# Kernel optimization log

Measured on AMD Instinct MI355X. Metric: run time of the kernel, lower is better.

## Reference

```python
import jax, jax.numpy as jnp
import numpy as np

N_HEADS = 16


def setup_inputs() -> dict:
    key = jax.random.key(0)
    ks = jax.random.split(key, 4)
    B, S, E = 4, 2048, 1024
    x = jax.random.normal(ks[0], (B, S, E), dtype=jnp.float32)
    w_attn = jax.random.normal(ks[1], (E, 3 * E), dtype=jnp.float32) * 0.02
    b_attn = jnp.zeros((3 * E,), dtype=jnp.float32)
    w_proj = jax.random.normal(ks[2], (E, E), dtype=jnp.float32) * 0.02
    b_proj = jnp.zeros((E,), dtype=jnp.float32)
    return {"x": x, "w_attn": w_attn, "b_attn": b_attn, "w_proj": w_proj, "b_proj": b_proj}


def reference(x, w_attn, b_attn, w_proj, b_proj):
    B, S, E = x.shape
    H = N_HEADS
    D = E // H
    # fused QKV projection (Conv1D: x @ W + b)
    qkv = x @ w_attn + b_attn                     # [B, S, 3E]
    q, k, v = jnp.split(qkv, 3, axis=-1)          # each [B, S, E]
    q = q.reshape(B, S, H, D).transpose(0, 2, 1, 3)  # [B, H, S, D]
    k = k.reshape(B, S, H, D).transpose(0, 2, 1, 3)
    v = v.reshape(B, S, H, D).transpose(0, 2, 1, 3)
    # scaled QK^T
    scores = jnp.einsum('bhqd,bhkd->bhqk', q, k) / jnp.sqrt(jnp.asarray(D, dtype=x.dtype))
    # causal mask via where with dtype-min fill (matches torch.where(c_m, w, finfo.min))
    causal = jnp.tril(jnp.ones((S, S), dtype=bool))  # [S, S]
    scores = jnp.where(causal[None, None, :, :], scores, jnp.finfo(scores.dtype).min)
    attn = jax.nn.softmax(scores, axis=-1)        # [B, H, S, S]
    o = jnp.einsum('bhqk,bhkd->bhqd', attn, v)    # [B, H, S, D]
    o = o.transpose(0, 2, 1, 3).reshape(B, S, E)  # merge heads
    return o @ w_proj + b_proj                    # output projection
```

## Files before the change

kernel.cpp:

```cpp
#include <hip/hip_runtime.h>
#include <stdint.h>


typedef __bf16 bf16;
typedef __bf16 bf16x4 __attribute__((ext_vector_type(4)));
typedef __bf16 bf16x8 __attribute__((ext_vector_type(8)));
typedef float  f32x4  __attribute__((ext_vector_type(4)));

#define DEV __device__ __forceinline__

DEV void async_copy16(bf16* lds, const bf16* g) {
  __builtin_amdgcn_global_load_lds(
      (__attribute__((address_space(1))) void*)(uintptr_t)g,
      (__attribute__((address_space(3))) void*)(uint32_t)(uintptr_t)lds,
      16, 0, 0);
}

__global__ __launch_bounds__(256) void cast_x_kernel(const float* __restrict__ in,
                                                     bf16* __restrict__ out, int n4) {
  int i = blockIdx.x * blockDim.x + threadIdx.x;
  int stride = gridDim.x * blockDim.x;
  for (; i < n4; i += stride) {
    float4 v = ((const float4*)in)[i];
    bf16x4 o = { (bf16)v.x, (bf16)v.y, (bf16)v.z, (bf16)v.w };
    *(bf16x4*)(out + (size_t)i * 4) = o;
  }
}

__global__ __launch_bounds__(256) void transpose_cast_kernel(const float* __restrict__ W,
                                                             bf16* __restrict__ Wt,
                                                             int Kd, int Nd) {
  __shared__ alignas(16) bf16 T[64 * 80];
  const int t = threadIdx.x;
  const int n0 = blockIdx.x * 64;
  const int k0 = blockIdx.y * 64;
#pragma unroll
  for (int i = 0; i < 4; ++i) {
    int idx = t + i * 256;
    int r  = idx >> 4;
    int c4 = (idx & 15) * 4;
    float4 v = *(const float4*)(W + (size_t)(k0 + r) * Nd + n0 + c4);
    bf16x4 o = { (bf16)v.x, (bf16)v.y, (bf16)v.z, (bf16)v.w };
    *(bf16x4*)(&T[r * 80 + c4]) = o;
  }
  __syncthreads();
#pragma unroll
  for (int i = 0; i < 2; ++i) {
    int idx = t + i * 256;
    int n = idx >> 3;
    int c = idx & 7;
    bf16x8 o;
#pragma unroll
    for (int j = 0; j < 8; ++j) o[j] = T[(c * 8 + j) * 80 + n];
    *(bf16x8*)(Wt + (size_t)(n0 + n) * Kd + k0 + c * 8) = o;
  }
}

__global__ __launch_bounds__(256) void vtrans_kernel(const bf16* __restrict__ qkv,
                                                     bf16* __restrict__ vt) {
  __shared__ alignas(16) bf16 T[64 * 80];
  const int t  = threadIdx.x;
  const int s0 = blockIdx.x * 64;
  const int bh = blockIdx.y;
  const int b = bh >> 4, h = bh & 15;
#pragma unroll
  for (int i = 0; i < 2; ++i) {
    int idx = t + i * 256;
    int s = idx >> 3, c = idx & 7;
    bf16x8 v = *(const bf16x8*)(qkv + (size_t)(b * 2048 + s0 + s) * 3072 + 2048 + h * 64 + c * 8);
    *(bf16x8*)(&T[s * 80 + c * 8]) = v;
  }
  __syncthreads();
#pragma unroll
  for (int i = 0; i < 2; ++i) {
    int idx = t + i * 256;
    int d = idx >> 3, c = idx & 7;
    bf16x8 o;
#pragma unroll
    for (int j = 0; j < 8; ++j) {
      int pos = c * 8 + j;
      int key = (pos & 32) | (((pos >> 2) & 1) << 4) | (((pos >> 3) & 3) << 2) | (pos & 3);
      o[j] = T[key * 80 + d];
    }
    *(bf16x8*)(vt + (size_t)(bh * 64 + d) * 2048 + s0 + c * 8) = o;
  }
}

template <typename OutT>
__global__ __launch_bounds__(512, 4) void gemm256_kernel(const bf16* __restrict__ A,
                                                         const bf16* __restrict__ Bt,
                                                         const float* __restrict__ bias,
                                                         OutT* __restrict__ C,
                                                         int M, int N, int K,
                                                         float qscale, int qcols,
                                                         int nbx) {
  __shared__ alignas(16) bf16 As[3][256 * 32];
  __shared__ alignas(16) bf16 Bs[3][128 * 32];

  const int tid  = threadIdx.x;
  const int lane = tid & 63;
  const int w    = tid >> 6;
  const int wm = w >> 1, wn = w & 1;
  const int l15 = lane & 15, l16 = lane >> 4;

  const int nwg = (int)gridDim.x;
  const int cpx = nwg >> 3;
  const int swz = ((int)blockIdx.x & 7) * cpx + ((int)blockIdx.x >> 3);
  const int m0 = (swz / nbx) * 256;
  const int n0 = (swz % nbx) * 128;

  const int c0  = w * 64 + lane;
  const int rA0 = c0 >> 2, sA0 = c0 & 3;
  const int rA1 = rA0 + 128;
  const bf16* srcA0 = A  + (size_t)(m0 + rA0) * K + 8 * (sA0 ^ ((rA0 >> 1) & 3));
  const bf16* srcA1 = A  + (size_t)(m0 + rA1) * K + 8 * (sA0 ^ ((rA1 >> 1) & 3));
  const bf16* srcB  = Bt + (size_t)(n0 + rA0) * K + 8 * (sA0 ^ ((rA0 >> 1) & 3));

#define STAGE_TILE(buf, kt)                                       \
  {                                                               \
    const int k0_ = (kt) * 32;                                    \
    async_copy16(&As[buf][(w * 64) * 8],         srcA0 + k0_);    \
    async_copy16(&As[buf][(512 + w * 64) * 8],   srcA1 + k0_);    \
    async_copy16(&Bs[buf][(w * 64) * 8],         srcB  + k0_);    \
  }

  f32x4 acc[4][4];
  f32x4 zf = {0.f, 0.f, 0.f, 0.f};
#pragma unroll
  for (int i = 0; i < 4; ++i)
#pragma unroll
    for (int j = 0; j < 4; ++j) acc[i][j] = zf;

  const int KT = K >> 5;
  STAGE_TILE(0, 0)
  STAGE_TILE(1, 1)

  const int soff = 8 * (l16 ^ ((l15 >> 1) & 3));

  int bufc = 0;
  int bufs = 2;
  for (int kt = 0; kt < KT; ++kt) {
    if (kt < KT - 1) { asm volatile("s_waitcnt vmcnt(3)" ::: "memory"); }
    else             { asm volatile("s_waitcnt vmcnt(0)" ::: "memory"); }
    __builtin_amdgcn_s_barrier();
    asm volatile("" ::: "memory");
    if (kt + 2 < KT) STAGE_TILE(bufs, kt + 2)

    bf16x8 bfr[4], afr[4];
#pragma unroll
    for (int n = 0; n < 4; ++n) {
      int rb = wn * 64 + n * 16 + l15;
      bfr[n] = *(const bf16x8*)(&Bs[bufc][rb * 32 + soff]);
    }
#pragma unroll
    for (int m = 0; m < 4; ++m) {
      int ra = wm * 64 + m * 16 + l15;
      afr[m] = *(const bf16x8*)(&As[bufc][ra * 32 + soff]);
    }
    __builtin_amdgcn_s_setprio(1);
#pragma unroll
    for (int m = 0; m < 4; ++m)
#pragma unroll
      for (int n = 0; n < 4; ++n)
        acc[m][n] = __builtin_amdgcn_mfma_f32_16x16x32_bf16(afr[m], bfr[n], acc[m][n], 0, 0, 0);
    __builtin_amdgcn_s_setprio(0);
    asm volatile("" ::: "memory");
    bufc = (bufc == 2) ? 0 : bufc + 1;
    bufs = (bufs == 2) ? 0 : bufs + 1;
  }

#pragma unroll
  for (int n = 0; n < 4; ++n) {
    int col = n0 + wn * 64 + n * 16 + l15;
    float bb = bias[col];
    float sc2 = (col < qcols) ? qscale : 1.0f;
#pragma unroll
    for (int m = 0; m < 4; ++m) {
#pragma unroll
      for (int reg = 0; reg < 4; ++reg) {
        int row = m0 + wm * 64 + m * 16 + l16 * 4 + reg;
        C[(size_t)row * N + col] = (OutT)((acc[m][n][reg] + bb) * sc2);
      }
    }
  }
#undef STAGE_TILE
}

__global__ __launch_bounds__(512, 4) void flash_kernel(const bf16* __restrict__ qkv,
                                                       const bf16* __restrict__ vt,
                                                       bf16* __restrict__ obuf) {
  constexpr int S = 2048, E3 = 3072;
  __shared__ alignas(16) bf16 Ks[2][64 * 64];
  __shared__ alignas(16) bf16 Vs[2][64 * 64];

  const int tid  = threadIdx.x;
  const int lane = tid & 63;
  const int w    = tid >> 6;
  const int bx = blockIdx.x;
  const int bh = blockIdx.y;
  const int b = bh >> 4, h = bh & 15;
  const int l15 = lane & 15, l16 = lane >> 4;

  const int sr  = w * 8 + (lane >> 3);
  const int scc = lane & 7;
  const bf16* kstage = qkv + (size_t)(b * S + sr) * E3 + 1024 + h * 64 + 8 * (scc ^ (sr & 7));
  const bf16* vstage = vt + (size_t)(bh * 64 + sr) * S + 8 * (scc ^ (sr & 7));

  const int xsw = l15 & 7;
  const uint32_t rdA = (uint32_t)(l15 * 128 + 16 * (l16 ^ xsw));
  const uint32_t rdB = (uint32_t)(l15 * 128 + 16 * ((4 + l16) ^ xsw));

#define KV_STAGE(buf, kv0_)                                        \
  {                                                                \
    async_copy16(Ks[buf] + w * 512, kstage + (size_t)(kv0_) * E3); \
    async_copy16(Vs[buf] + w * 512, vstage + (kv0_));              \
  }

  for (int half = 0; half < 2; ++half) {
    const int t = half ? (15 - bx) : bx;
    const int q0 = t * 128;
    const int wq0 = q0 + w * 16;
    const int nsteps = 2 * t + 2;

    KV_STAGE(0, 0)

    bf16x8 qf[2];
    {
      const bf16* qbase = qkv + (size_t)(b * S + wq0 + l15) * E3 + h * 64;
#pragma unroll
      for (int dk = 0; dk < 2; ++dk)
        qf[dk] = *(const bf16x8*)(qbase + (dk * 4 + l16) * 8);
    }

    float lstate = 0.f;
    f32x4 oacc[4];
    f32x4 zf = {0.f, 0.f, 0.f, 0.f};
#pragma unroll
    for (int i = 0; i < 4; ++i) oacc[i] = zf;

    __syncthreads();

#define FLASH_STEP(CUR, STEPIDX)                                                  \
    {                                                                             \
      const int kv0 = (STEPIDX) * 64;                                             \
      if ((STEPIDX) + 1 < nsteps) KV_STAGE((CUR) ^ 1, kv0 + 64)                   \
      if (kv0 <= wq0 + 15) {                     \
        f32x4 sv[4];                                                              \
        _Pragma("unroll")                                                         \
        for (int kf = 0; kf < 4; ++kf) sv[kf] = zf;                               \
        __builtin_amdgcn_s_setprio(1);                                            \
        _Pragma("unroll")                                                         \
        for (int kf = 0; kf < 4; ++kf) {                                          \
          bf16x8 k0 = *(const bf16x8*)((const char*)Ks[CUR] + rdA + kf * 2048);   \
          sv[kf] = __builtin_amdgcn_mfma_f32_16x16x32_bf16(k0, qf[0], sv[kf], 0, 0, 0); \
          bf16x8 k1 = *(const bf16x8*)((const char*)Ks[CUR] + rdB + kf * 2048);   \
          sv[kf] = __builtin_amdgcn_mfma_f32_16x16x32_bf16(k1, qf[1], sv[kf], 0, 0, 0); \
        }                                                                         \
        __builtin_amdgcn_s_setprio(0);                                            \
        if (kv0 + 63 > wq0) {     \
          const int qrow_ = wq0 + l15;                                            \
          _Pragma("unroll")                                                       \
          for (int kf = 0; kf < 4; ++kf)                                          \
            _Pragma("unroll")                                                     \
            for (int reg = 0; reg < 4; ++reg) {                                   \
              int key = kv0 + kf * 16 + l16 * 4 + reg;                            \
              if (key > qrow_) sv[kf][reg] = -1e30f;                              \
            }                                                                     \
        }                                                                         \
        float rsum = 0.f;                                                         \
        _Pragma("unroll")                                                         \
        for (int kf = 0; kf < 4; ++kf)                                            \
          _Pragma("unroll")                                                       \
          for (int reg = 0; reg < 4; ++reg) {                                     \
            float p = __builtin_amdgcn_exp2f(sv[kf][reg]);                        \
            sv[kf][reg] = p;                                                      \
            rsum += p;                                                            \
          }                                                                       \
        rsum += __shfl_xor(rsum, 16);                                             \
        rsum += __shfl_xor(rsum, 32);                                             \
        lstate += rsum;                                                           \
             \
        bf16x8 pb[2];                                                             \
        _Pragma("unroll")                                                         \
        for (int kc = 0; kc < 2; ++kc) {                                          \
          bf16x8 tq;                                                              \
          tq[0] = (bf16)sv[2 * kc][0];  tq[1] = (bf16)sv[2 * kc][1];              \
          tq[2] = (bf16)sv[2 * kc][2];  tq[3] = (bf16)sv[2 * kc][3];              \
          tq[4] = (bf16)sv[2 * kc + 1][0]; tq[5] = (bf16)sv[2 * kc + 1][1];       \
          tq[6] = (bf16)sv[2 * kc + 1][2]; tq[7] = (bf16)sv[2 * kc + 1][3];       \
          pb[kc] = tq;                                                            \
        }                                                                         \
        __builtin_amdgcn_s_setprio(1);                                            \
        _Pragma("unroll")                                                         \
        for (int nf = 0; nf < 4; ++nf) {                                          \
          bf16x8 vf0 = *(const bf16x8*)((const char*)Vs[CUR] + rdA + nf * 2048);  \
          oacc[nf] = __builtin_amdgcn_mfma_f32_16x16x32_bf16(vf0, pb[0], oacc[nf], 0, 0, 0); \
          bf16x8 vf1 = *(const bf16x8*)((const char*)Vs[CUR] + rdB + nf * 2048);  \
          oacc[nf] = __builtin_amdgcn_mfma_f32_16x16x32_bf16(vf1, pb[1], oacc[nf], 0, 0, 0); \
        }                                                                         \
        __builtin_amdgcn_s_setprio(0);                                            \
      }                                                                           \
      __syncthreads();          \
    }

    for (int step = 0; step < nsteps; step += 2) {
      FLASH_STEP(0, step)
      FLASH_STEP(1, step + 1)
    }
#undef FLASH_STEP

    float inv = 1.0f / lstate;
    int qrow = wq0 + l15;
#pragma unroll
    for (int nf = 0; nf < 4; ++nf) {
      bf16x4 o4 = { (bf16)(oacc[nf][0] * inv), (bf16)(oacc[nf][1] * inv),
                    (bf16)(oacc[nf][2] * inv), (bf16)(oacc[nf][3] * inv) };
      *(bf16x4*)(obuf + (size_t)(b * S + qrow) * 1024 + h * 64 + nf * 16 + l16 * 4) = o4;
    }
  }
#undef KV_STAGE
}

extern "C" void kernel_launch(void* const* d_in, const int* in_sizes, int n_in,
                              void* d_out, int out_size, void* d_ws, size_t ws_size,
                              hipStream_t stream) {
  (void)in_sizes; (void)n_in; (void)out_size; (void)ws_size;
  const float* x      = (const float*)d_in[0];
  const float* w_attn = (const float*)d_in[1];
  const float* b_attn = (const float*)d_in[2];
  const float* w_proj = (const float*)d_in[3];
  const float* b_proj = (const float*)d_in[4];
  float* out = (float*)d_out;

  char* ws = (char*)d_ws;
  bf16* xb  = (bf16*)(ws + 0);
  bf16* wat = (bf16*)(ws + 16777216);
  bf16* wpt = (bf16*)(ws + 23068672);
  bf16* qkv = (bf16*)(ws + 25165824);
  bf16* vt  = (bf16*)(ws + 75497472);
  bf16* ob  = (bf16*)(ws + 92274688);

  const float QSCALE = 0.18033688011112042f;

  cast_x_kernel<<<2048, 256, 0, stream>>>(x, xb, 8192 * 1024 / 4);
  transpose_cast_kernel<<<dim3(48, 16), 256, 0, stream>>>(w_attn, wat, 1024, 3072);
  transpose_cast_kernel<<<dim3(16, 16), 256, 0, stream>>>(w_proj, wpt, 1024, 1024);
  gemm256_kernel<bf16><<<768, 512, 0, stream>>>(xb, wat, b_attn, qkv,
                                                8192, 3072, 1024, QSCALE, 1024, 24);
  vtrans_kernel<<<dim3(32, 64), 256, 0, stream>>>(qkv, vt);
  flash_kernel<<<dim3(8, 64), 512, 0, stream>>>(qkv, vt, ob);
  gemm256_kernel<float><<<256, 512, 0, stream>>>(ob, wpt, b_proj, out,
                                                 8192, 1024, 1024, 1.0f, 0, 8);
}
```

Baseline: 160.8 us.

## Double query rows per flash wave to reuse K/V tiles across two sub-tiles

Each flash block now covers 256 query rows, with every wave handling two 16-row query sub-tiles against the same K/V LDS tiles. Each K/V load and barrier is amortized over twice the MFMA work, and the grid is halved. In exchange, register pressure rises (launch bounds lowered to 2 blocks/CU), occupancy falls, and causal tail waste per block grows.

```diff
diff --git a/kernel.cpp b/kernel.cpp
--- a/kernel.cpp
+++ b/kernel.cpp
@@ -186,7 +186,7 @@
 #undef STAGE_TILE
 }
 
-__global__ __launch_bounds__(512, 4) void flash_kernel(const bf16* __restrict__ qkv,
+__global__ __launch_bounds__(512, 2) void flash_kernel(const bf16* __restrict__ qkv,
                                                        const bf16* __restrict__ vt,
                                                        bf16* __restrict__ obuf) {
   constexpr int S = 2048, E3 = 3072;
@@ -217,26 +217,30 @@
   }
 
   for (int half = 0; half < 2; ++half) {
-    const int t = half ? (15 - bx) : bx;
-    const int q0 = t * 128;
-    const int wq0 = q0 + w * 16;
-    const int nsteps = 2 * t + 2;
+    const int t = half ? (7 - bx) : bx;
+    const int q0 = t * 256;
+    const int wq0 = q0 + w * 32;
+    const int nsteps = 4 * t + 4;
 
     KV_STAGE(0, 0)
 
-    bf16x8 qf[2];
+    bf16x8 qf[2][2];
     {
-      const bf16* qbase = qkv + (size_t)(b * S + wq0 + l15) * E3 + h * 64;
-#pragma unroll
-      for (int dk = 0; dk < 2; ++dk)
-        qf[dk] = *(const bf16x8*)(qbase + (dk * 4 + l16) * 8);
-    }
-
-    float lstate = 0.f;
-    f32x4 oacc[4];
+      const bf16* qbase = qkv + (size_t)(b * S + wq0) * E3 + h * 64;
+#pragma unroll
+      for (int s = 0; s < 2; ++s)
+#pragma unroll
+        for (int dk = 0; dk < 2; ++dk)
+          qf[s][dk] = *(const bf16x8*)(qbase + (size_t)(s * 16 + l15) * E3 + (dk * 4 + l16) * 8);
+    }
+
+    float lstate[2] = {0.f, 0.f};
+    f32x4 oacc[2][4];
     f32x4 zf = {0.f, 0.f, 0.f, 0.f};
 #pragma unroll
-    for (int i = 0; i < 4; ++i) oacc[i] = zf;
+    for (int s = 0; s < 2; ++s)
+#pragma unroll
+      for (int i = 0; i < 4; ++i) oacc[s][i] = zf;
 
     __syncthreads();
 
@@ -244,59 +248,65 @@
     {                                                                             \
       const int kv0 = (STEPIDX) * 64;                                             \
       if ((STEPIDX) + 1 < nsteps) KV_STAGE((CUR) ^ 1, kv0 + 64)                   \
-      if (kv0 <= wq0 + 15) {                     \
-        f32x4 sv[4];                                                              \
+      if (kv0 <= wq0 + 31) {                     \
+        f32x4 sv[2][4];                                                           \
         _Pragma("unroll")                                                         \
-        for (int kf = 0; kf < 4; ++kf) sv[kf] = zf;                               \
+        for (int kf = 0; kf < 4; ++kf) { sv[0][kf] = zf; sv[1][kf] = zf; }        \
         __builtin_amdgcn_s_setprio(1);                                            \
         _Pragma("unroll")                                                         \
         for (int kf = 0; kf < 4; ++kf) {                                          \
           bf16x8 k0 = *(const bf16x8*)((const char*)Ks[CUR] + rdA + kf * 2048);   \
-          sv[kf] = __builtin_amdgcn_mfma_f32_16x16x32_bf16(k0, qf[0], sv[kf], 0, 0, 0); \
+          sv[0][kf] = __builtin_amdgcn_mfma_f32_16x16x32_bf16(k0, qf[0][0], sv[0][kf], 0, 0, 0); \
+          sv[1][kf] = __builtin_amdgcn_mfma_f32_16x16x32_bf16(k0, qf[1][0], sv[1][kf], 0, 0, 0); \
           bf16x8 k1 = *(const bf16x8*)((const char*)Ks[CUR] + rdB + kf * 2048);   \
-          sv[kf] = __builtin_amdgcn_mfma_f32_16x16x32_bf16(k1, qf[1], sv[kf], 0, 0, 0); \
+          sv[0][kf] = __builtin_amdgcn_mfma_f32_16x16x32_bf16(k1, qf[0][1], sv[0][kf], 0, 0, 0); \
+          sv[1][kf] = __builtin_amdgcn_mfma_f32_16x16x32_bf16(k1, qf[1][1], sv[1][kf], 0, 0, 0); \
         }                                                                         \
         __builtin_amdgcn_s_setprio(0);                                            \
-        if (kv0 + 63 > wq0) {     \
-          const int qrow_ = wq0 + l15;                                            \
+        bf16x8 pb[2][2];                                                          \
+        _Pragma("unroll")                                                         \
+        for (int s = 0; s < 2; ++s) {                                             \
+          if (kv0 + 63 > wq0 + s * 16) {                \
+            const int qrow_ = wq0 + s * 16 + l15;                                 \
+            _Pragma("unroll")                                                     \
+            for (int kf = 0; kf < 4; ++kf)                                        \
+              _Pragma("unroll")                                                   \
+              for (int reg = 0; reg < 4; ++reg) {                                 \
+                int key = kv0 + kf * 16 + l16 * 4 + reg;                          \
+                if (key > qrow_) sv[s][kf][reg] = -1e30f;                         \
+              }                                                                   \
+          }                                                                       \
+          float rsum = 0.f;                                                       \
           _Pragma("unroll")                                                       \
           for (int kf = 0; kf < 4; ++kf)                                          \
             _Pragma("unroll")                                                     \
             for (int reg = 0; reg < 4; ++reg) {                                   \
-              int key = kv0 + kf * 16 + l16 * 4 + reg;                            \
-              if (key > qrow_) sv[kf][reg] = -1e30f;                              \
+              float p = __builtin_amdgcn_exp2f(sv[s][kf][reg]);                   \
+              sv[s][kf][reg] = p;                                                 \
+              rsum += p;                                                          \
             }                                                                     \
-        }                                                                         \
-        float rsum = 0.f;                                                         \
-        _Pragma("unroll")                                                         \
-        for (int kf = 0; kf < 4; ++kf)                                            \
+          rsum += __shfl_xor(rsum, 16);                                           \
+          rsum += __shfl_xor(rsum, 32);                                           \
+          lstate[s] += rsum;                                                      \
           _Pragma("unroll")                                                       \
-          for (int reg = 0; reg < 4; ++reg) {                                     \
-            float p = __builtin_amdgcn_exp2f(sv[kf][reg]);                        \
-            sv[kf][reg] = p;                                                      \
-            rsum += p;                                                            \
+          for (int kc = 0; kc < 2; ++kc) {                                        \
+            bf16x8 tq;                                                            \
+            tq[0] = (bf16)sv[s][2 * kc][0];  tq[1] = (bf16)sv[s][2 * kc][1];      \
+            tq[2] = (bf16)sv[s][2 * kc][2];  tq[3] = (bf16)sv[s][2 * kc][3];      \
+            tq[4] = (bf16)sv[s][2 * kc + 1][0]; tq[5] = (bf16)sv[s][2 * kc + 1][1]; \
+            tq[6] = (bf16)sv[s][2 * kc + 1][2]; tq[7] = (bf16)sv[s][2 * kc + 1][3]; \
+            pb[s][kc] = tq;                                                       \
           }                                                                       \
-        rsum += __shfl_xor(rsum, 16);                                             \
-        rsum += __shfl_xor(rsum, 32);                                             \
-        lstate += rsum;                                                           \
-             \
-        bf16x8 pb[2];                                                             \
-        _Pragma("unroll")                                                         \
-        for (int kc = 0; kc < 2; ++kc) {                                          \
-          bf16x8 tq;                                                              \
-          tq[0] = (bf16)sv[2 * kc][0];  tq[1] = (bf16)sv[2 * kc][1];              \
-          tq[2] = (bf16)sv[2 * kc][2];  tq[3] = (bf16)sv[2 * kc][3];              \
-          tq[4] = (bf16)sv[2 * kc + 1][0]; tq[5] = (bf16)sv[2 * kc + 1][1];       \
-          tq[6] = (bf16)sv[2 * kc + 1][2]; tq[7] = (bf16)sv[2 * kc + 1][3];       \
-          pb[kc] = tq;                                                            \
         }                                                                         \
         __builtin_amdgcn_s_setprio(1);                                            \
         _Pragma("unroll")                                                         \
         for (int nf = 0; nf < 4; ++nf) {                                          \
           bf16x8 vf0 = *(const bf16x8*)((const char*)Vs[CUR] + rdA + nf * 2048);  \
-          oacc[nf] = __builtin_amdgcn_mfma_f32_16x16x32_bf16(vf0, pb[0], oacc[nf], 0, 0, 0); \
+          oacc[0][nf] = __builtin_amdgcn_mfma_f32_16x16x32_bf16(vf0, pb[0][0], oacc[0][nf], 0, 0, 0); \
+          oacc[1][nf] = __builtin_amdgcn_mfma_f32_16x16x32_bf16(vf0, pb[1][0], oacc[1][nf], 0, 0, 0); \
           bf16x8 vf1 = *(const bf16x8*)((const char*)Vs[CUR] + rdB + nf * 2048);  \
-          oacc[nf] = __builtin_amdgcn_mfma_f32_16x16x32_bf16(vf1, pb[1], oacc[nf], 0, 0, 0); \
+          oacc[0][nf] = __builtin_amdgcn_mfma_f32_16x16x32_bf16(vf1, pb[0][1], oacc[0][nf], 0, 0, 0); \
+          oacc[1][nf] = __builtin_amdgcn_mfma_f32_16x16x32_bf16(vf1, pb[1][1], oacc[1][nf], 0, 0, 0); \
         }                                                                         \
         __builtin_amdgcn_s_setprio(0);                                            \
       }                                                                           \
@@ -309,13 +319,16 @@
     }
 #undef FLASH_STEP
 
-    float inv = 1.0f / lstate;
-    int qrow = wq0 + l15;
-#pragma unroll
-    for (int nf = 0; nf < 4; ++nf) {
-      bf16x4 o4 = { (bf16)(oacc[nf][0] * inv), (bf16)(oacc[nf][1] * inv),
-                    (bf16)(oacc[nf][2] * inv), (bf16)(oacc[nf][3] * inv) };
-      *(bf16x4*)(obuf + (size_t)(b * S + qrow) * 1024 + h * 64 + nf * 16 + l16 * 4) = o4;
+#pragma unroll
+    for (int s = 0; s < 2; ++s) {
+      float inv = 1.0f / lstate[s];
+      int qrow = wq0 + s * 16 + l15;
+#pragma unroll
+      for (int nf = 0; nf < 4; ++nf) {
+        bf16x4 o4 = { (bf16)(oacc[s][nf][0] * inv), (bf16)(oacc[s][nf][1] * inv),
+                      (bf16)(oacc[s][nf][2] * inv), (bf16)(oacc[s][nf][3] * inv) };
+        *(bf16x4*)(obuf + (size_t)(b * S + qrow) * 1024 + h * 64 + nf * 16 + l16 * 4) = o4;
+      }
     }
   }
 #undef KV_STAGE
@@ -348,7 +361,7 @@
   gemm256_kernel<bf16><<<768, 512, 0, stream>>>(xb, wat, b_attn, qkv,
                                                 8192, 3072, 1024, QSCALE, 1024, 24);
   vtrans_kernel<<<dim3(32, 64), 256, 0, stream>>>(qkv, vt);
-  flash_kernel<<<dim3(8, 64), 512, 0, stream>>>(qkv, vt, ob);
+  flash_kernel<<<dim3(4, 64), 512, 0, stream>>>(qkv, vt, ob);
   gemm256_kernel<float><<<256, 512, 0, stream>>>(ob, wpt, b_proj, out,
                                                  8192, 1024, 1024, 1.0f, 0, 8);
 }
```

After: 160.7 us. No clear change (-0.1%).
